# Performance work log

Hardware: AMD Instinct MI355X
Metric: run time of the kernel (lower is better)

The kernel has to match this reference:

```python
import jax, jax.numpy as jnp
import numpy as np


def setup_inputs() -> dict:
    key = jax.random.key(0)
    k1, k2 = jax.random.split(key)
    B, C, H, W = 4, 128, 192, 640
    left = jax.random.normal(k1, (B, C, H, W), dtype=jnp.float32)
    right = jax.random.normal(k2, (B, C, H, W), dtype=jnp.float32)
    return {"left": left, "right": right, "num_disparities": 96}


def reference(left, right, num_disparities):
    """Dot-product stereo cost volume (is_right=False).

    cost[b, d, y, x] = sum_c left[b, c, y, x] * right[b, c, y, x - d],
    with zeros where x - d < 0.  Output: [B, D, H, W].
    """
    D = num_disparities
    B, C, H, W = left.shape
    # Zero-pad right on the left edge of the width axis so that the slice
    # starting at (D-1-d) gives right shifted by d with zero fill.
    right_pad = jnp.pad(right, ((0, 0), (0, 0), (0, 0), (D - 1, 0)))

    def per_disparity(d):
        r = jax.lax.dynamic_slice_in_dim(right_pad, (D - 1) - d, W, axis=3)
        return jnp.sum(left * r, axis=1)  # [B, H, W], reduce over channels

    cost = jax.lax.map(per_disparity, jnp.arange(D))  # [D, B, H, W]
    return jnp.transpose(cost, (1, 0, 2, 3))  # [B, D, H, W]
```

## Files before the change

kernel.cpp:

```cpp
#include <hip/hip_runtime.h>

#define Bn 4
#define Cn 128
#define Hn 192
#define Wn 640
#define Dn 96
#define HW (Hn * Wn)

#define PRh 40
#define PLh 40
#define EP 68

typedef float f32x4 __attribute__((ext_vector_type(4)));
typedef short short8 __attribute__((ext_vector_type(8)));
typedef unsigned short ushort8 __attribute__((ext_vector_type(8)));

__device__ __forceinline__ unsigned short f2bf(float f) {
  unsigned int u = __builtin_bit_cast(unsigned int, f);
  u += 0x7FFFu + ((u >> 16) & 1u);
  return (unsigned short)(u >> 16);
}

union SMem {
  struct {
    unsigned short R[160 * PRh];
    unsigned short L[64 * PLh];
  } s;
  float epi[48 * EP];
};

__global__ __launch_bounds__(256, 5) void cost_volume_kernel(
    const float* __restrict__ left, const float* __restrict__ right,
    float* __restrict__ out) {
  __shared__ SMem sm;

  const int x0 = blockIdx.x * 64;
  const int y  = blockIdx.y;
  const int b  = blockIdx.z;
  const int t  = threadIdx.x;
  const int w  = t >> 6;
  const int l  = t & 63;
  const int n  = t & 15;
  const int q  = (t >> 4) & 3;

  f32x4 acc[7];
#pragma unroll
  for (int jj = 0; jj < 7; ++jj) acc[jj] = (f32x4){0.f, 0.f, 0.f, 0.f};

  const float* lrow = left  + ((size_t)(b * Cn) * Hn + y) * Wn + x0;
  const float* rrow = right + ((size_t)(b * Cn) * Hn + y) * Wn + x0 - 96;

  float rv[3][8];
  float lv[8];
  auto load_chunk = [&](int ck) {
    const float* rb = rrow + (size_t)(ck + 8 * w) * HW;
#pragma unroll
    for (int i = 0; i < 3; ++i) {
      const int u = l + 64 * i;
      const bool ok = (u < 160) && (x0 + u >= 96);
#pragma unroll
      for (int j = 0; j < 8; ++j) rv[i][j] = ok ? rb[(size_t)j * HW + u] : 0.f;
    }
    const float* lb = lrow + (size_t)(ck + 8 * w) * HW;
#pragma unroll
    for (int j = 0; j < 8; ++j) lv[j] = lb[(size_t)j * HW + l];
  };

  load_chunk(0);
#pragma unroll
  for (int kk = 0; kk < 4; ++kk) {
    __syncthreads();
#pragma unroll
    for (int i = 0; i < 3; ++i) {
      const int u = l + 64 * i;
      if (u < 160) {
        ushort8 pk;
#pragma unroll
        for (int j = 0; j < 8; ++j) pk[j] = f2bf(rv[i][j]);
        *(ushort8*)&sm.s.R[u * PRh + 8 * w] = pk;
      }
    }
    {
      ushort8 pl;
#pragma unroll
      for (int j = 0; j < 8; ++j) pl[j] = f2bf(lv[j]);
      *(ushort8*)&sm.s.L[l * PLh + 8 * w] = pl;
    }
    __syncthreads();
    if (kk < 3) load_chunk(32 * (kk + 1));

    {
      const short8 bf = *(const short8*)&sm.s.L[(16 * w + n) * PLh + 8 * q];
#pragma unroll
      for (int jj = 0; jj < 7; ++jj) {
        const short8 af =
            *(const short8*)&sm.s.R[(16 * w + 16 * jj + n) * PRh + 8 * q];
        acc[jj] = __builtin_amdgcn_mfma_f32_16x16x32_bf16(af, bf, acc[jj], 0, 0, 0);
      }
    }
  }

#pragma unroll
  for (int p = 0; p < 2; ++p) {
    __syncthreads();
#pragma unroll
    for (int jj = 0; jj < 7; ++jj)
#pragma unroll
      for (int r = 0; r < 4; ++r) {
        const int d = 96 + n - 16 * jj - 4 * q - r - 48 * p;
        if (d >= 0 && d < 48) sm.epi[d * EP + 16 * w + n] = acc[jj][r];
      }
    __syncthreads();
    const size_t obase = (((size_t)b * Dn + 48 * p) * Hn + y) * Wn + x0;
    const int tx = (t & 15) << 2;
    const int d0 = t >> 4;
#pragma unroll
    for (int ii = 0; ii < 3; ++ii) {
      const int d = d0 + 16 * ii;
      f32x4 v = *(const f32x4*)&sm.epi[d * EP + tx];
      *(f32x4*)&out[obase + (size_t)d * HW + tx] = v;
    }
  }
}

extern "C" void kernel_launch(void* const* d_in, const int* in_sizes, int n_in,
                              void* d_out, int out_size, void* d_ws, size_t ws_size,
                              hipStream_t stream) {
  const float* left  = (const float*)d_in[0];
  const float* right = (const float*)d_in[1];
  float* out = (float*)d_out;
  dim3 grid(Wn / 64, Hn, Bn);
  cost_volume_kernel<<<grid, dim3(256, 1, 1), 0, stream>>>(left, right, out);
}
```

Before: 554.2 us.

## Double-buffer global loads, swizzle block order, and single-pass epilogue

Global loads now use two register buffers so each chunk is fetched two stages ahead of its shared-memory store. The explicit barriers use sched_barrier to stop the compiler from reordering work across them. Block indices are swizzled so neighbouring dispatch slots (likely spread across XCDs) map to contiguous work. The epilogue writes all 96 disparities in one pass through a larger shared buffer. Launch bounds drop from 5 to 4 waves per SIMD to make room for the extra registers and LDS, which costs occupancy.

```diff
diff --git a/kernel.cpp b/kernel.cpp
--- a/kernel.cpp
+++ b/kernel.cpp
@@ -26,22 +26,34 @@
     unsigned short R[160 * PRh];
     unsigned short L[64 * PLh];
   } s;
-  float epi[48 * EP];
+  float epi[96 * EP];
 };
 
-__global__ __launch_bounds__(256, 5) void cost_volume_kernel(
+#define LGKM0() asm volatile("s_waitcnt lgkmcnt(0)" ::: "memory")
+#define SBAR()                         \
+  do {                                 \
+    __builtin_amdgcn_sched_barrier(0); \
+    __builtin_amdgcn_s_barrier();      \
+    __builtin_amdgcn_sched_barrier(0); \
+  } while (0)
+
+__global__ __launch_bounds__(256, 4) void cost_volume_kernel(
     const float* __restrict__ left, const float* __restrict__ right,
     float* __restrict__ out) {
   __shared__ SMem sm;
 
-  const int x0 = blockIdx.x * 64;
-  const int y  = blockIdx.y;
-  const int b  = blockIdx.z;
-  const int t  = threadIdx.x;
-  const int w  = t >> 6;
-  const int l  = t & 63;
-  const int n  = t & 15;
-  const int q  = (t >> 4) & 3;
+  const int orig = blockIdx.x + 10 * (blockIdx.y + 192 * blockIdx.z);
+  const int swz  = (orig & 7) * 960 + (orig >> 3);
+  const int x0 = (swz % 10) * 64;
+  const int yb = swz / 10;
+  const int y  = yb % 192;
+  const int b  = yb / 192;
+
+  const int t = threadIdx.x;
+  const int w = t >> 6;
+  const int l = t & 63;
+  const int n = t & 15;
+  const int q = (t >> 4) & 3;
 
   f32x4 acc[7];
 #pragma unroll
@@ -50,76 +62,87 @@
   const float* lrow = left  + ((size_t)(b * Cn) * Hn + y) * Wn + x0;
   const float* rrow = right + ((size_t)(b * Cn) * Hn + y) * Wn + x0 - 96;
 
-  float rv[3][8];
-  float lv[8];
-  auto load_chunk = [&](int ck) {
-    const float* rb = rrow + (size_t)(ck + 8 * w) * HW;
+  float ra[24], la[8], rb[24], lb[8];
+
+  auto load_chunk = [&](float (&rv)[24], float (&lv)[8], int ck) {
+    const float* rbp = rrow + (size_t)(ck + 8 * w) * HW;
 #pragma unroll
     for (int i = 0; i < 3; ++i) {
       const int u = l + 64 * i;
       const bool ok = (u < 160) && (x0 + u >= 96);
 #pragma unroll
-      for (int j = 0; j < 8; ++j) rv[i][j] = ok ? rb[(size_t)j * HW + u] : 0.f;
+      for (int j = 0; j < 8; ++j) rv[i * 8 + j] = ok ? rbp[(size_t)j * HW + u] : 0.f;
     }
-    const float* lb = lrow + (size_t)(ck + 8 * w) * HW;
+    const float* lbp = lrow + (size_t)(ck + 8 * w) * HW;
 #pragma unroll
-    for (int j = 0; j < 8; ++j) lv[j] = lb[(size_t)j * HW + l];
+    for (int j = 0; j < 8; ++j) lv[j] = lbp[(size_t)j * HW + l];
   };
 
-  load_chunk(0);
-#pragma unroll
-  for (int kk = 0; kk < 4; ++kk) {
-    __syncthreads();
+  auto store_chunk = [&](float (&rv)[24], float (&lv)[8]) {
 #pragma unroll
     for (int i = 0; i < 3; ++i) {
       const int u = l + 64 * i;
       if (u < 160) {
         ushort8 pk;
 #pragma unroll
-        for (int j = 0; j < 8; ++j) pk[j] = f2bf(rv[i][j]);
+        for (int j = 0; j < 8; ++j) pk[j] = f2bf(rv[i * 8 + j]);
         *(ushort8*)&sm.s.R[u * PRh + 8 * w] = pk;
       }
     }
-    {
-      ushort8 pl;
+    ushort8 pl;
 #pragma unroll
-      for (int j = 0; j < 8; ++j) pl[j] = f2bf(lv[j]);
-      *(ushort8*)&sm.s.L[l * PLh + 8 * w] = pl;
+    for (int j = 0; j < 8; ++j) pl[j] = f2bf(lv[j]);
+    *(ushort8*)&sm.s.L[l * PLh + 8 * w] = pl;
+  };
+
+  auto mfma_phase = [&]() {
+    const short8 bf = *(const short8*)&sm.s.L[(16 * w + n) * PLh + 8 * q];
+#pragma unroll
+    for (int jj = 0; jj < 7; ++jj) {
+      const short8 af =
+          *(const short8*)&sm.s.R[(16 * w + 16 * jj + n) * PRh + 8 * q];
+      acc[jj] = __builtin_amdgcn_mfma_f32_16x16x32_bf16(af, bf, acc[jj], 0, 0, 0);
     }
-    __syncthreads();
-    if (kk < 3) load_chunk(32 * (kk + 1));
+  };
 
-    {
-      const short8 bf = *(const short8*)&sm.s.L[(16 * w + n) * PLh + 8 * q];
+  load_chunk(ra, la, 0);
+  load_chunk(rb, lb, 32);
+
+  store_chunk(ra, la);
+  load_chunk(ra, la, 64);
+  LGKM0(); SBAR();
+  mfma_phase();
+  LGKM0(); SBAR();
+  store_chunk(rb, lb);
+  load_chunk(rb, lb, 96);
+  LGKM0(); SBAR();
+  mfma_phase();
+  LGKM0(); SBAR();
+  store_chunk(ra, la);
+  LGKM0(); SBAR();
+  mfma_phase();
+  LGKM0(); SBAR();
+  store_chunk(rb, lb);
+  LGKM0(); SBAR();
+  mfma_phase();
+
+  __syncthreads();
 #pragma unroll
-      for (int jj = 0; jj < 7; ++jj) {
-        const short8 af =
-            *(const short8*)&sm.s.R[(16 * w + 16 * jj + n) * PRh + 8 * q];
-        acc[jj] = __builtin_amdgcn_mfma_f32_16x16x32_bf16(af, bf, acc[jj], 0, 0, 0);
-      }
+  for (int jj = 0; jj < 7; ++jj)
+#pragma unroll
+    for (int r = 0; r < 4; ++r) {
+      const int d = 96 + n - 16 * jj - 4 * q - r;
+      if (d >= 0 && d < 96) sm.epi[d * EP + 16 * w + n] = acc[jj][r];
     }
-  }
-
+  __syncthreads();
+  const size_t obase = ((size_t)b * Dn * Hn + y) * (size_t)Wn + x0;
+  const int tx = (t & 15) << 2;
+  const int d0 = t >> 4;
 #pragma unroll
-  for (int p = 0; p < 2; ++p) {
-    __syncthreads();
-#pragma unroll
-    for (int jj = 0; jj < 7; ++jj)
-#pragma unroll
-      for (int r = 0; r < 4; ++r) {
-        const int d = 96 + n - 16 * jj - 4 * q - r - 48 * p;
-        if (d >= 0 && d < 48) sm.epi[d * EP + 16 * w + n] = acc[jj][r];
-      }
-    __syncthreads();
-    const size_t obase = (((size_t)b * Dn + 48 * p) * Hn + y) * Wn + x0;
-    const int tx = (t & 15) << 2;
-    const int d0 = t >> 4;
-#pragma unroll
-    for (int ii = 0; ii < 3; ++ii) {
-      const int d = d0 + 16 * ii;
-      f32x4 v = *(const f32x4*)&sm.epi[d * EP + tx];
-      *(f32x4*)&out[obase + (size_t)d * HW + tx] = v;
-    }
+  for (int ii = 0; ii < 6; ++ii) {
+    const int d = d0 + 16 * ii;
+    f32x4 v = *(const f32x4*)&sm.epi[d * EP + tx];
+    *(f32x4*)&out[obase + (size_t)d * HW + tx] = v;
   }
 }
 
```

Result: no change. 546.6 us (-1.4%).
